# Kernel optimization log

Measured on AMD Instinct MI355X. Metric: run time of the kernel, lower is better.

## Reference

```python
import jax, jax.numpy as jnp
import numpy as np

HIDDEN = 128
HEADS = 8
HEAD_DIM = HIDDEN // HEADS
N_BLOCKS = 2048
N_EDGES = 4096


def setup_inputs() -> dict:
    key = jax.random.key(0)
    ks = jax.random.split(key, 14)
    s = 0.02
    return {
        "block_features": jax.random.normal(ks[0], (N_BLOCKS, HIDDEN), dtype=jnp.float32),
        "edge_indices": jax.random.randint(ks[1], (2, N_EDGES), 0, N_BLOCKS, dtype=jnp.int32),
        # edge_encoder: Linear(2H->H), ReLU, Linear(H->H)
        "W_e1": jax.random.normal(ks[2], (2 * HIDDEN, HIDDEN), dtype=jnp.float32) * s,
        "b_e1": jnp.zeros((HIDDEN,), dtype=jnp.float32),
        "W_e2": jax.random.normal(ks[3], (HIDDEN, HIDDEN), dtype=jnp.float32) * s,
        "b_e2": jnp.zeros((HIDDEN,), dtype=jnp.float32),
        "Wq": jax.random.normal(ks[4], (HIDDEN, HIDDEN), dtype=jnp.float32) * s,
        "bq": jnp.zeros((HIDDEN,), dtype=jnp.float32),
        "Wk": jax.random.normal(ks[5], (HIDDEN, HIDDEN), dtype=jnp.float32) * s,
        "bk": jnp.zeros((HIDDEN,), dtype=jnp.float32),
        "Wv": jax.random.normal(ks[6], (HIDDEN, HIDDEN), dtype=jnp.float32) * s,
        "bv": jnp.zeros((HIDDEN,), dtype=jnp.float32),
        "Wo": jax.random.normal(ks[7], (HIDDEN, HIDDEN), dtype=jnp.float32) * s,
        "bo": jnp.zeros((HIDDEN,), dtype=jnp.float32),
    }


def reference(block_features, edge_indices, W_e1, b_e1, W_e2, b_e2,
              Wq, bq, Wk, bk, Wv, bv, Wo, bo):
    n_blocks = block_features.shape[0]
    src_idx, dst_idx = edge_indices[0], edge_indices[1]

    # gather src/dst node features, concat -> edge MLP (dropout is identity in eval)
    ef = jnp.concatenate([block_features[src_idx], block_features[dst_idx]], axis=1)  # [E, 2H]
    ef = jnp.maximum(ef @ W_e1 + b_e1, 0.0) @ W_e2 + b_e2  # [E, H]

    E = ef.shape[0]
    scale = HEAD_DIM ** -0.5
    q = (ef @ Wq + bq).reshape(E, HEADS, HEAD_DIM)
    k = (ef @ Wk + bk).reshape(E, HEADS, HEAD_DIM)
    v = (ef @ Wv + bv).reshape(E, HEADS, HEAD_DIM)

    # dense attention over all edges
    scores = jnp.einsum("ehd,fhd->hef", q, k) * scale  # [H, E, E]
    attn = jax.nn.softmax(scores, axis=-1)
    attn_out = jnp.einsum("hef,fhd->ehd", attn, v).reshape(E, HIDDEN)
    updated_edges = attn_out @ Wo + bo  # [E, H]

    # scatter_sum back to destination nodes
    block_updates = jax.ops.segment_sum(updated_edges, dst_idx, num_segments=n_blocks)
    return block_features + block_updates
```

## Files before the change

### kernel.cpp

```cpp
#include <hip/hip_runtime.h>
#include <hip/hip_bf16.h>

#define NB 2048
#define NE 4096
#define HID 128
#define NHEAD 8
#define HD 16

#define FPSCALE 1048576.0f
#define INV_FPSCALE (1.0f/1048576.0f)
#define QSCALE 0.36067376022224085f

typedef short s16x8 __attribute__((ext_vector_type(8)));
typedef float f32x4  __attribute__((ext_vector_type(4)));
typedef float f32x16 __attribute__((ext_vector_type(16)));

static __device__ __forceinline__ ushort f2bf(float x) {
    uint u = __builtin_bit_cast(uint, x);
    uint r = (u + 0x7fffu + ((u >> 16) & 1u)) >> 16;
    return (ushort)r;
}
static __device__ __forceinline__ uint pack2bf(float a, float b) {
    return (uint)f2bf(a) | ((uint)f2bf(b) << 16);
}
static __device__ __forceinline__ uint packrd(float a, float b) {
    uint ua = __builtin_bit_cast(uint, a) + 0x8000u;
    uint ub = __builtin_bit_cast(uint, b) + 0x8000u;
    return __builtin_amdgcn_perm(ub, ua, 0x07060302u);
}

__global__ __launch_bounds__(256) void convert_kernel(
    const float* __restrict__ We1, const float* __restrict__ We2,
    const float* __restrict__ Wq,  const float* __restrict__ Wk,
    const float* __restrict__ Wv,  const float* __restrict__ Wo,
    ushort* __restrict__ wb, int4* __restrict__ acc_zero)
{
    int i = blockIdx.x * 256 + threadIdx.x;
    if (i < 65536) acc_zero[i] = make_int4(0, 0, 0, 0);
    if (i < 32768) {
        int n = i >> 8, k = i & 255;
        wb[i] = f2bf(We1[k * HID + n]);
        return;
    }
    int j = i - 32768;
    int m = j >> 14;
    int r = j & 16383;
    int n = r >> 7, k = r & 127;
    const float* W = (m == 0) ? We2 : (m == 1) ? Wq : (m == 2) ? Wk : (m == 3) ? Wv : Wo;
    wb[i] = f2bf(W[k * HID + n]);
}

__global__ __launch_bounds__(512) void mlp_qkv_kernel(
    const float* __restrict__ bf, const int* __restrict__ src, const int* __restrict__ dst,
    const ushort* __restrict__ wb,
    const float* __restrict__ be1, const float* __restrict__ be2,
    const float* __restrict__ bq,  const float* __restrict__ bk, const float* __restrict__ bv,
    ushort* __restrict__ qg, ushort* __restrict__ kg, ushort* __restrict__ vT)
{
    __shared__ ushort sX[16][264];
    __shared__ ushort sH[16][136];
    __shared__ ushort sE[16][136];

    const int tid = threadIdx.x;
    const int w   = tid >> 6;
    const int l   = tid & 63;
    const int lo16 = l & 15;
    const int hi4  = l >> 4;
    const int e0 = blockIdx.x * 16;

    const ushort* We1T = wb;
    const ushort* We2T = wb + 32768;
    const ushort* WqT  = wb + 49152;
    const ushort* WkT  = wb + 65536;
    const ushort* WvT  = wb + 81920;

    {
        const int r  = tid >> 5;
        const int sg = tid & 31;
        const int e  = e0 + r;
        const int node = (sg < 16) ? src[e] : dst[e];
        const float4* rowp = (const float4*)(bf + node * HID);
        const int fb = (sg & 15) * 2;
        float4 t0 = rowp[fb], t1 = rowp[fb + 1];
        *(uint2*)&sX[r][sg * 8]     = make_uint2(pack2bf(t0.x, t0.y), pack2bf(t0.z, t0.w));
        *(uint2*)&sX[r][sg * 8 + 4] = make_uint2(pack2bf(t1.x, t1.y), pack2bf(t1.z, t1.w));
    }
    __syncthreads();

    f32x4 acc;

    {
        float b = be1[w * 16 + lo16];
        acc = (f32x4){b, b, b, b};
        #pragma unroll
        for (int k0 = 0; k0 < 8; k0++) {
            s16x8 a = *(const s16x8*)&sX[lo16][k0 * 32 + hi4 * 8];
            s16x8 bb = *(const s16x8*)(We1T + (w * 16 + lo16) * 256 + k0 * 32 + hi4 * 8);
            acc = __builtin_amdgcn_mfma_f32_16x16x32_bf16(a, bb, acc, 0, 0, 0);
        }
        #pragma unroll
        for (int r = 0; r < 4; r++)
            sH[hi4 * 4 + r][w * 16 + lo16] = f2bf(fmaxf(acc[r], 0.0f));
    }
    __syncthreads();

    {
        float b = be2[w * 16 + lo16];
        acc = (f32x4){b, b, b, b};
        #pragma unroll
        for (int k0 = 0; k0 < 4; k0++) {
            s16x8 a = *(const s16x8*)&sH[lo16][k0 * 32 + hi4 * 8];
            s16x8 bb = *(const s16x8*)(We2T + (w * 16 + lo16) * 128 + k0 * 32 + hi4 * 8);
            acc = __builtin_amdgcn_mfma_f32_16x16x32_bf16(a, bb, acc, 0, 0, 0);
        }
        #pragma unroll
        for (int r = 0; r < 4; r++)
            sE[hi4 * 4 + r][w * 16 + lo16] = f2bf(acc[r]);
    }
    __syncthreads();

#define PROJ(WT, BIAS, STORE) do { \
    float b_ = BIAS[w * 16 + lo16]; \
    acc = (f32x4){b_, b_, b_, b_}; \
    _Pragma("unroll") \
    for (int k0 = 0; k0 < 4; k0++) { \
        s16x8 a = *(const s16x8*)&sE[lo16][k0 * 32 + hi4 * 8]; \
        s16x8 bb = *(const s16x8*)(WT + (w * 16 + lo16) * 128 + k0 * 32 + hi4 * 8); \
        acc = __builtin_amdgcn_mfma_f32_16x16x32_bf16(a, bb, acc, 0, 0, 0); \
    } \
    _Pragma("unroll") \
    for (int r = 0; r < 4; r++) { STORE; } \
} while (0)

    PROJ(WqT, bq, { int e = e0 + hi4 * 4 + r;
                    qg[(w * NE + e) * 16 + lo16] = f2bf(acc[r] * QSCALE); });
    PROJ(WkT, bk, { int e = e0 + hi4 * 4 + r;
                    kg[(w * NE + e) * 16 + lo16] = f2bf(acc[r]); });
    PROJ(WvT, bv, { int e = e0 + hi4 * 4 + r;
                    vT[(w * 16 + lo16) * NE + e] = f2bf(acc[r]); });
#undef PROJ
}

__global__ __launch_bounds__(256) void attn_kernel(
    const ushort* __restrict__ qg, const ushort* __restrict__ kg,
    const ushort* __restrict__ vT, ushort* __restrict__ Og)
{
    __shared__ ushort P[4][2][8][32][4];
    __shared__ float sO[4][32][18];

    const int tid = threadIdx.x;
    const int w   = tid >> 6;
    const int l   = tid & 63;
    const int h   = blockIdx.y;
    const int q0  = blockIdx.x * 32;
    const int lo16 = l & 15, hi4 = l >> 4;
    const int lo32 = l & 31, hi2 = l >> 5;

    const s16x8 qf = *(const s16x8*)(qg + (h * NE + q0 + lo32) * 16 + hi2 * 8);
    const s16x8 ones = __builtin_bit_cast(s16x8,
        make_uint4(0x3f803f80u, 0x3f803f80u, 0x3f803f80u, 0x3f803f80u));

    const f32x16 z16 = {};
    f32x4 o0 = {0,0,0,0}, o1 = {0,0,0,0};
    f32x4 l0 = {0,0,0,0}, l1 = {0,0,0,0};

    const int kbase = w * (NE / 4);

    #pragma unroll 2
    for (int kt = 0; kt < NE / 4 / 32; kt++) {
        const int key0 = kbase + kt * 32;
        const int b = kt & 1;
        s16x8 kf = *(const s16x8*)(kg + (h * NE + key0 + lo32) * 16 + hi2 * 8);
        s16x8 vf = *(const s16x8*)(vT + (h * 16 + lo16) * NE + key0 + hi4 * 8);

        f32x16 s = __builtin_amdgcn_mfma_f32_32x32x16_bf16(kf, qf, z16, 0, 0, 0);

        #pragma unroll
        for (int g = 0; g < 4; g++) {
            uint2 w2 = make_uint2(
                packrd(__builtin_amdgcn_exp2f(s[4*g]),   __builtin_amdgcn_exp2f(s[4*g+1])),
                packrd(__builtin_amdgcn_exp2f(s[4*g+2]), __builtin_amdgcn_exp2f(s[4*g+3])));
            *(uint2*)&P[w][b][2*g + hi2][lo32][0] = w2;
        }

        uint2 alo = *(const uint2*)&P[w][b][2*hi4][lo16][0];
        uint2 ahi = *(const uint2*)&P[w][b][2*hi4 + 1][lo16][0];
        uint2 blo = *(const uint2*)&P[w][b][2*hi4][16 + lo16][0];
        uint2 bhi = *(const uint2*)&P[w][b][2*hi4 + 1][16 + lo16][0];
        s16x8 pb0 = __builtin_bit_cast(s16x8, make_uint4(alo.x, alo.y, ahi.x, ahi.y));
        s16x8 pb1 = __builtin_bit_cast(s16x8, make_uint4(blo.x, blo.y, bhi.x, bhi.y));

        o0 = __builtin_amdgcn_mfma_f32_16x16x32_bf16(vf, pb0, o0, 0, 0, 0);
        o1 = __builtin_amdgcn_mfma_f32_16x16x32_bf16(vf, pb1, o1, 0, 0, 0);
        l0 = __builtin_amdgcn_mfma_f32_16x16x32_bf16(ones, pb0, l0, 0, 0, 0);
        l1 = __builtin_amdgcn_mfma_f32_16x16x32_bf16(ones, pb1, l1, 0, 0, 0);
    }

    #pragma unroll
    for (int r = 0; r < 4; r++) {
        sO[w][lo16][hi4 * 4 + r]      = o0[r];
        sO[w][16 + lo16][hi4 * 4 + r] = o1[r];
    }
    if (hi4 == 0) {
        sO[w][lo16][16]      = l0[0];
        sO[w][16 + lo16][16] = l1[0];
    }
    __syncthreads();

    {
        const int q = tid >> 3;
        const int d0 = (tid & 7) * 2;
        float s0 = 0.0f, s1 = 0.0f, Lq = 0.0f;
        #pragma unroll
        for (int ww = 0; ww < 4; ww++) {
            s0 += sO[ww][q][d0];
            s1 += sO[ww][q][d0 + 1];
            Lq += sO[ww][q][16];
        }
        float inv = 1.0f / Lq;
        *(uint*)&Og[(q0 + q) * HID + h * 16 + d0] = pack2bf(s0 * inv, s1 * inv);
    }
}

__global__ __launch_bounds__(512) void wo_scatter_kernel(
    const ushort* __restrict__ Og, const ushort* __restrict__ wb,
    const float* __restrict__ bo, const int* __restrict__ dst,
    int* __restrict__ acc_int)
{
    const int tid = threadIdx.x;
    const int w   = tid >> 6;
    const int l   = tid & 63;
    const int lo16 = l & 15, hi4 = l >> 4;
    const int e0 = blockIdx.x * 16;
    const ushort* WoT = wb + 98304;

    float b_ = bo[w * 16 + lo16];
    f32x4 acc = (f32x4){b_, b_, b_, b_};
    #pragma unroll
    for (int k0 = 0; k0 < 4; k0++) {
        s16x8 a = *(const s16x8*)(Og + (e0 + lo16) * HID + k0 * 32 + hi4 * 8);
        s16x8 bb = *(const s16x8*)(WoT + (w * 16 + lo16) * 128 + k0 * 32 + hi4 * 8);
        acc = __builtin_amdgcn_mfma_f32_16x16x32_bf16(a, bb, acc, 0, 0, 0);
    }

    #pragma unroll
    for (int r = 0; r < 4; r++) {
        int n = dst[e0 + hi4 * 4 + r];
        atomicAdd(acc_int + n * HID + w * 16 + lo16,
                  __float2int_rn(acc[r] * FPSCALE));
    }
}

__global__ __launch_bounds__(256) void finalize_kernel(
    const float4* __restrict__ bf, const int4* __restrict__ acc_int,
    float4* __restrict__ out)
{
    int i = blockIdx.x * 256 + threadIdx.x;
    float4 b = bf[i];
    int4   a = acc_int[i];
    out[i] = make_float4(b.x + (float)a.x * INV_FPSCALE,
                         b.y + (float)a.y * INV_FPSCALE,
                         b.z + (float)a.z * INV_FPSCALE,
                         b.w + (float)a.w * INV_FPSCALE);
}

extern "C" void kernel_launch(void* const* d_in, const int* in_sizes, int n_in,
                              void* d_out, int out_size, void* d_ws, size_t ws_size,
                              hipStream_t stream)
{
    const float* bf  = (const float*)d_in[0];
    const int*   ei  = (const int*)d_in[1];
    const int*   src = ei;
    const int*   dst = ei + NE;
    const float* We1 = (const float*)d_in[2];
    const float* be1 = (const float*)d_in[3];
    const float* We2 = (const float*)d_in[4];
    const float* be2 = (const float*)d_in[5];
    const float* Wq  = (const float*)d_in[6];
    const float* bq  = (const float*)d_in[7];
    const float* Wk  = (const float*)d_in[8];
    const float* bk  = (const float*)d_in[9];
    const float* Wv  = (const float*)d_in[10];
    const float* bv  = (const float*)d_in[11];
    const float* Wo  = (const float*)d_in[12];
    const float* bo  = (const float*)d_in[13];

    char* ws = (char*)d_ws;
    ushort* wb  = (ushort*)(ws);
    ushort* qg  = (ushort*)(ws + (1u<<18));
    ushort* kg  = (ushort*)(ws + (1u<<18) + (1u<<20));
    ushort* vT  = (ushort*)(ws + (1u<<18) + (2u<<20));
    ushort* Og  = (ushort*)(ws + (1u<<18) + (3u<<20));
    int*   acc  = (int*)  (ws + (1u<<18) + (4u<<20));

    convert_kernel<<<448, 256, 0, stream>>>(We1, We2, Wq, Wk, Wv, Wo, wb, (int4*)acc);
    mlp_qkv_kernel<<<NE / 16, 512, 0, stream>>>(bf, src, dst, wb, be1, be2, bq, bk, bv,
                                                qg, kg, vT);
    attn_kernel<<<dim3(NE / 32, NHEAD), 256, 0, stream>>>(qg, kg, vT, Og);
    wo_scatter_kernel<<<NE / 16, 512, 0, stream>>>(Og, wb, bo, dst, acc);
    finalize_kernel<<<(NB * HID) / 1024, 256, 0, stream>>>((const float4*)bf, (const int4*)acc,
                                                           (float4*)d_out);
}
```

Measured before the change: 55.31 us.

## Split attention keys across 8 waves and software-prefetch K/V fragments

The attention kernel now runs 512 threads per block, so each of 8 waves covers 512 keys instead of 1024, which doubles the waves in flight for the same grid. The K and V fragments for the next key tile are loaded one iteration ahead to hide global-load latency behind the MFMA and exp work. The per-wave P buffer is reused as the reduction buffer, with an added barrier, to keep LDS use down. The final reduction now sums 8 partials with one output element per thread, and the last iteration issues one redundant wraparound prefetch.

```diff
diff --git a/kernel.cpp b/kernel.cpp
--- a/kernel.cpp
+++ b/kernel.cpp
@@ -141,12 +141,11 @@
 #undef PROJ
 }
 
-__global__ __launch_bounds__(256) void attn_kernel(
+__global__ __launch_bounds__(512) void attn_kernel(
     const ushort* __restrict__ qg, const ushort* __restrict__ kg,
     const ushort* __restrict__ vT, ushort* __restrict__ Og)
 {
-    __shared__ ushort P[4][2][8][32][4];
-    __shared__ float sO[4][32][18];
+    __shared__ ushort Pbuf[8][2048];
 
     const int tid = threadIdx.x;
     const int w   = tid >> 6;
@@ -156,6 +155,8 @@
     const int lo16 = l & 15, hi4 = l >> 4;
     const int lo32 = l & 31, hi2 = l >> 5;
 
+    ushort* Pw = &Pbuf[w][0];
+
     const s16x8 qf = *(const s16x8*)(qg + (h * NE + q0 + lo32) * 16 + hi2 * 8);
     const s16x8 ones = __builtin_bit_cast(s16x8,
         make_uint4(0x3f803f80u, 0x3f803f80u, 0x3f803f80u, 0x3f803f80u));
@@ -164,61 +165,67 @@
     f32x4 o0 = {0,0,0,0}, o1 = {0,0,0,0};
     f32x4 l0 = {0,0,0,0}, l1 = {0,0,0,0};
 
-    const int kbase = w * (NE / 4);
+    const int kbase = w * (NE / 8);
+    const ushort* kp = kg + (size_t)h * NE * 16;
+    const ushort* vp = vT + (size_t)(h * 16 + lo16) * NE;
+
+    s16x8 kf = *(const s16x8*)(kp + (kbase + lo32) * 16 + hi2 * 8);
+    s16x8 vf = *(const s16x8*)(vp + kbase + hi4 * 8);
 
     #pragma unroll 2
-    for (int kt = 0; kt < NE / 4 / 32; kt++) {
-        const int key0 = kbase + kt * 32;
-        const int b = kt & 1;
-        s16x8 kf = *(const s16x8*)(kg + (h * NE + key0 + lo32) * 16 + hi2 * 8);
-        s16x8 vf = *(const s16x8*)(vT + (h * 16 + lo16) * NE + key0 + hi4 * 8);
-
-        f32x16 s = __builtin_amdgcn_mfma_f32_32x32x16_bf16(kf, qf, z16, 0, 0, 0);
-
+    for (int kt = 0; kt < 16; kt++) {
+        const s16x8 kc = kf, vc = vf;
+        const int key1 = kbase + ((kt + 1) & 15) * 32;
+        kf = *(const s16x8*)(kp + (key1 + lo32) * 16 + hi2 * 8);
+        vf = *(const s16x8*)(vp + key1 + hi4 * 8);
+
+        f32x16 s = __builtin_amdgcn_mfma_f32_32x32x16_bf16(kc, qf, z16, 0, 0, 0);
+
+        const int b8 = (kt & 1) * 8;
         #pragma unroll
         for (int g = 0; g < 4; g++) {
             uint2 w2 = make_uint2(
                 packrd(__builtin_amdgcn_exp2f(s[4*g]),   __builtin_amdgcn_exp2f(s[4*g+1])),
                 packrd(__builtin_amdgcn_exp2f(s[4*g+2]), __builtin_amdgcn_exp2f(s[4*g+3])));
-            *(uint2*)&P[w][b][2*g + hi2][lo32][0] = w2;
+            *(uint2*)&Pw[((b8 + 2*g + hi2) * 32 + lo32) * 4] = w2;
         }
 
-        uint2 alo = *(const uint2*)&P[w][b][2*hi4][lo16][0];
-        uint2 ahi = *(const uint2*)&P[w][b][2*hi4 + 1][lo16][0];
-        uint2 blo = *(const uint2*)&P[w][b][2*hi4][16 + lo16][0];
-        uint2 bhi = *(const uint2*)&P[w][b][2*hi4 + 1][16 + lo16][0];
+        uint2 alo = *(const uint2*)&Pw[((b8 + 2*hi4)     * 32 + lo16) * 4];
+        uint2 ahi = *(const uint2*)&Pw[((b8 + 2*hi4 + 1) * 32 + lo16) * 4];
+        uint2 blo = *(const uint2*)&Pw[((b8 + 2*hi4)     * 32 + 16 + lo16) * 4];
+        uint2 bhi = *(const uint2*)&Pw[((b8 + 2*hi4 + 1) * 32 + 16 + lo16) * 4];
         s16x8 pb0 = __builtin_bit_cast(s16x8, make_uint4(alo.x, alo.y, ahi.x, ahi.y));
         s16x8 pb1 = __builtin_bit_cast(s16x8, make_uint4(blo.x, blo.y, bhi.x, bhi.y));
 
-        o0 = __builtin_amdgcn_mfma_f32_16x16x32_bf16(vf, pb0, o0, 0, 0, 0);
-        o1 = __builtin_amdgcn_mfma_f32_16x16x32_bf16(vf, pb1, o1, 0, 0, 0);
+        o0 = __builtin_amdgcn_mfma_f32_16x16x32_bf16(vc, pb0, o0, 0, 0, 0);
+        o1 = __builtin_amdgcn_mfma_f32_16x16x32_bf16(vc, pb1, o1, 0, 0, 0);
         l0 = __builtin_amdgcn_mfma_f32_16x16x32_bf16(ones, pb0, l0, 0, 0, 0);
         l1 = __builtin_amdgcn_mfma_f32_16x16x32_bf16(ones, pb1, l1, 0, 0, 0);
     }
 
+    __syncthreads();
+    float* sO = (float*)&Pbuf[0][0];
     #pragma unroll
     for (int r = 0; r < 4; r++) {
-        sO[w][lo16][hi4 * 4 + r]      = o0[r];
-        sO[w][16 + lo16][hi4 * 4 + r] = o1[r];
+        sO[(w * 32 + lo16) * 18 + hi4 * 4 + r]      = o0[r];
+        sO[(w * 32 + 16 + lo16) * 18 + hi4 * 4 + r] = o1[r];
     }
     if (hi4 == 0) {
-        sO[w][lo16][16]      = l0[0];
-        sO[w][16 + lo16][16] = l1[0];
+        sO[(w * 32 + lo16) * 18 + 16]      = l0[0];
+        sO[(w * 32 + 16 + lo16) * 18 + 16] = l1[0];
     }
     __syncthreads();
 
     {
-        const int q = tid >> 3;
-        const int d0 = (tid & 7) * 2;
-        float s0 = 0.0f, s1 = 0.0f, Lq = 0.0f;
-        #pragma unroll
-        for (int ww = 0; ww < 4; ww++) {
-            s0 += sO[ww][q][d0];
-            s1 += sO[ww][q][d0 + 1];
-            Lq += sO[ww][q][16];
+        const int q = tid >> 4;
+        const int d = tid & 15;
+        float sum = 0.0f, Lq = 0.0f;
+        #pragma unroll
+        for (int ww = 0; ww < 8; ww++) {
+            sum += sO[(ww * 32 + q) * 18 + d];
+            Lq  += sO[(ww * 32 + q) * 18 + 16];
         }
-        float inv = 1.0f / Lq;
-        *(uint*)&Og[(q0 + q) * HID + h * 16 + d0] = pack2bf(s0 * inv, s1 * inv);
+        Og[(q0 + q) * HID + h * 16 + d] = f2bf(sum / Lq);
     }
 }
 
@@ -296,7 +303,7 @@
     convert_kernel<<<448, 256, 0, stream>>>(We1, We2, Wq, Wk, Wv, Wo, wb, (int4*)acc);
     mlp_qkv_kernel<<<NE / 16, 512, 0, stream>>>(bf, src, dst, wb, be1, be2, bq, bk, bv,
                                                 qg, kg, vT);
-    attn_kernel<<<dim3(NE / 32, NHEAD), 256, 0, stream>>>(qg, kg, vT, Og);
+    attn_kernel<<<dim3(NE / 32, NHEAD), 512, 0, stream>>>(qg, kg, vT, Og);
     wo_scatter_kernel<<<NE / 16, 512, 0, stream>>>(Og, wb, bo, dst, acc);
     finalize_kernel<<<(NB * HID) / 1024, 256, 0, stream>>>((const float4*)bf, (const int4*)acc,
                                                            (float4*)d_out);
```

Result: faster. 52.74 us (-4.6%).
